# Optimization experiments

Hardware: AMD Instinct MI355X
Metric: run time of the kernel (lower is better)

Reference implementation:

```python
import jax, jax.numpy as jnp
import numpy as np

BATCH, DIN, DSTATE, SEQLEN = 4, 2048, 16, 2048


def setup_inputs() -> dict:
    key = jax.random.key(0)
    ks = jax.random.split(key, 7)
    u = jax.random.normal(ks[0], (BATCH, DIN, SEQLEN), dtype=jnp.float32)
    # delta pre-softplus; moderate positive-ish values like Mamba dt_proj output
    delta = jax.random.uniform(ks[1], (BATCH, DIN, SEQLEN), dtype=jnp.float32, minval=-2.0, maxval=1.0)
    # A is negative in real Mamba (A = -exp(A_log)); keep recurrence stable
    A = -jnp.exp(jax.random.uniform(ks[2], (DIN, DSTATE), dtype=jnp.float32, minval=-1.0, maxval=1.0))
    B = jax.random.normal(ks[3], (BATCH, DSTATE, SEQLEN), dtype=jnp.float32)
    C = jax.random.normal(ks[4], (BATCH, DSTATE, SEQLEN), dtype=jnp.float32)
    D = jax.random.normal(ks[5], (DIN,), dtype=jnp.float32)
    z = jax.random.normal(ks[6], (BATCH, DIN, SEQLEN), dtype=jnp.float32)
    return {"u": u, "delta": delta, "A": A, "B": B, "C": C, "D": D, "z": z}


def reference(u, delta, A, B, C, D, z):
    """Mamba selective scan (selective_scan_ref semantics, delta_softplus=True).

    u, delta, z: (b, d, l); A: (d, n); B, C: (b, n, l); D: (d,).
    y_t = C_t . x_t + D*u_t, x_t = exp(dt_t*A)*x_{t-1} + dt_t*B_t*u_t,
    final y gated by SiLU(z).
    """
    dt = jax.nn.softplus(delta)                      # (b, d, l)

    def step(x, inp):
        dt_t, u_t, B_t, C_t = inp                    # (b,d) (b,d) (b,n) (b,n)
        dA = jnp.exp(dt_t[..., None] * A)            # (b, d, n)
        x = x * dA + (dt_t * u_t)[..., None] * B_t[:, None, :]
        y_t = jnp.einsum('bdn,bn->bd', x, C_t)
        return x, y_t

    xs = (jnp.moveaxis(dt, -1, 0),                   # (l, b, d)
          jnp.moveaxis(u, -1, 0),
          jnp.moveaxis(B, -1, 0),                    # (l, b, n)
          jnp.moveaxis(C, -1, 0))
    x0 = jnp.zeros((u.shape[0], u.shape[1], A.shape[1]), dtype=u.dtype)
    _, ys = jax.lax.scan(step, x0, xs)               # ys: (l, b, d)
    y = jnp.moveaxis(ys, 0, -1)                      # (b, d, l)
    y = y + D[None, :, None] * u
    y = y * (z * jax.nn.sigmoid(z))                  # SiLU gate
    return y
```

## Files before the change

kernel.cpp:

```cpp
#include <hip/hip_runtime.h>


#define BATCHSZ 4
#define DIN 2048
#define NSTATE 16
#define SEQ 2048
#define NCH (BATCHSZ * DIN)
#define NGRP (NCH / 256)
#define TT 32
#define ST 36
#define L2E 1.44269504f

__device__ __forceinline__ float softplus_f(float v) {
    float e = __builtin_amdgcn_exp2f(v * L2E);
    return 0.69314718f * __builtin_amdgcn_logf(1.0f + e);
}

__device__ __forceinline__ float silu_f(float v) {
    float s = __builtin_amdgcn_rcpf(1.0f + __builtin_amdgcn_exp2f(-v * L2E));
    return v * s;
}

__device__ __forceinline__ float comp4(const float4& f, int k) {
    return k == 0 ? f.x : k == 1 ? f.y : k == 2 ? f.z : f.w;
}

__device__ __forceinline__ void set4(float4& f, int k, float v) {
    if (k == 0) f.x = v; else if (k == 1) f.y = v; else if (k == 2) f.z = v; else f.w = v;
}


template<int NC>
__global__ __launch_bounds__(256, 2) void k_pass1(
        const float* __restrict__ u, const float* __restrict__ delta,
        const float* __restrict__ A, const float* __restrict__ Bm,
        float* __restrict__ ws) {
    constexpr int LC = SEQ / NC;
    constexpr int NT = LC / TT;
    __shared__ float Ub[256 * ST];
    __shared__ float Db[256 * ST];
    __shared__ float Bc[LC * 20];

    int tid = threadIdx.x;
    int g = blockIdx.x & (NGRP - 1);
    int c = blockIdx.x >> 5;
    int chBase = g << 8;
    int b = chBase >> 11;
    int bd = chBase + tid;
    int d = bd & (DIN - 1);

    float A2[NSTATE];
    {
        const float* Ar = A + (size_t)d * NSTATE;
        #pragma unroll
        for (int n = 0; n < NSTATE; ++n) A2[n] = Ar[n] * L2E;
    }

    const float* ug = u + (size_t)chBase * SEQ + (size_t)c * LC;
    const float* dg = delta + (size_t)chBase * SEQ + (size_t)c * LC;
    const float* Bg = Bm + (size_t)b * NSTATE * SEQ + (size_t)c * LC;

    #pragma unroll
    for (int i = 0; i < LC * NSTATE / 256; ++i) {
        int e = i * 256 + tid;
        int n = e / LC;
        int t = e % LC;
        Bc[t * 20 + n] = Bg[(size_t)n * SEQ + t];
    }

    float x[NSTATE];
    #pragma unroll
    for (int n = 0; n < NSTATE; ++n) x[n] = 0.0f;
    float S = 0.0f;

    for (int tile = 0; tile < NT; ++tile) {
        int tb = tile * TT;
        __syncthreads();
        #pragma unroll
        for (int it = 0; it < 8; ++it) {
            int r = it * 32 + (tid >> 3), cq = (tid & 7) * 4;
            *(float4*)(&Ub[r * ST + cq]) = *(const float4*)(ug + (size_t)r * SEQ + tb + cq);
            *(float4*)(&Db[r * ST + cq]) = *(const float4*)(dg + (size_t)r * SEQ + tb + cq);
        }
        __syncthreads();
        #pragma unroll
        for (int t4 = 0; t4 < TT / 4; ++t4) {
            float4 u4 = *(const float4*)(&Ub[tid * ST + t4 * 4]);
            float4 d4 = *(const float4*)(&Db[tid * ST + t4 * 4]);
            #pragma unroll
            for (int k = 0; k < 4; ++k) {
                float dt = softplus_f(comp4(d4, k));
                S += dt;
                float du = dt * comp4(u4, k);
                int t = tb + t4 * 4 + k;
                const float4* Br = (const float4*)(&Bc[t * 20]);
                float bb[NSTATE];
                *(float4*)&bb[0] = Br[0]; *(float4*)&bb[4] = Br[1];
                *(float4*)&bb[8] = Br[2]; *(float4*)&bb[12] = Br[3];
                #pragma unroll
                for (int n = 0; n < NSTATE; ++n) {
                    float dA = __builtin_amdgcn_exp2f(A2[n] * dt);
                    x[n] = x[n] * dA + du * bb[n];
                }
            }
        }
    }

    float* wsq = ws;
    float* wsS = ws + (size_t)NSTATE * NC * NCH;
    #pragma unroll
    for (int n = 0; n < NSTATE; ++n) wsq[((size_t)n * NC + c) * NCH + bd] = x[n];
    wsS[(size_t)c * NCH + bd] = S;
}

template<int NC>
__global__ __launch_bounds__(256) void k_pass2(
        const float* __restrict__ A, float* __restrict__ ws) {
    int idx = blockIdx.x * 256 + threadIdx.x;
    int n = idx >> 13;
    int bd = idx & (NCH - 1);
    int d = bd & (DIN - 1);

    float A2 = A[(size_t)d * NSTATE + n] * L2E;
    float x = 0.0f;
    float* wsq = ws;
    float* wsS = ws + (size_t)NSTATE * NC * NCH;

    for (int c = 0; c < NC; ++c) {
        float S = wsS[(size_t)c * NCH + bd];
        float* p = wsq + ((size_t)n * NC + c) * NCH + bd;
        float q = *p;
        float P = __builtin_amdgcn_exp2f(A2 * S);
        *p = x;
        x = x * P + q;
    }
}

template<int NC>
__global__ __launch_bounds__(256, 2) void k_pass3(
        const float* __restrict__ u, const float* __restrict__ delta,
        const float* __restrict__ A, const float* __restrict__ Bm,
        const float* __restrict__ Cm, const float* __restrict__ Dv,
        const float* __restrict__ z, const float* __restrict__ ws,
        float* __restrict__ out) {
    constexpr int LC = SEQ / NC;
    constexpr int NT = LC / TT;
    __shared__ float Ub[256 * ST];
    __shared__ float Db[256 * ST];
    __shared__ float Bc[LC * 20];
    __shared__ float Cc[LC * 20];

    int tid = threadIdx.x;
    int g = blockIdx.x & (NGRP - 1);
    int c = blockIdx.x >> 5;
    int chBase = g << 8;
    int b = chBase >> 11;
    int bd = chBase + tid;
    int d = bd & (DIN - 1);

    float A2[NSTATE];
    {
        const float* Ar = A + (size_t)d * NSTATE;
        #pragma unroll
        for (int n = 0; n < NSTATE; ++n) A2[n] = Ar[n] * L2E;
    }

    const float* ug = u + (size_t)chBase * SEQ + (size_t)c * LC;
    const float* dg = delta + (size_t)chBase * SEQ + (size_t)c * LC;
    const float* zg = z + (size_t)chBase * SEQ + (size_t)c * LC;
    float* og = out + (size_t)chBase * SEQ + (size_t)c * LC;
    const float* Bg = Bm + (size_t)b * NSTATE * SEQ + (size_t)c * LC;
    const float* Cg = Cm + (size_t)b * NSTATE * SEQ + (size_t)c * LC;

    #pragma unroll
    for (int i = 0; i < LC * NSTATE / 256; ++i) {
        int e = i * 256 + tid;
        int n = e / LC;
        int t = e % LC;
        Bc[t * 20 + n] = Bg[(size_t)n * SEQ + t];
        Cc[t * 20 + n] = Cg[(size_t)n * SEQ + t];
    }

    const float* wsq = ws;
    float x[NSTATE];
    #pragma unroll
    for (int n = 0; n < NSTATE; ++n)
        x[n] = wsq[((size_t)n * NC + c) * NCH + bd];
    float Dd = Dv[d];

    for (int tile = 0; tile < NT; ++tile) {
        int tb = tile * TT;
        __syncthreads();
        float4 zr[8];
        #pragma unroll
        for (int it = 0; it < 8; ++it) {
            int r = it * 32 + (tid >> 3), cq = (tid & 7) * 4;
            *(float4*)(&Ub[r * ST + cq]) = *(const float4*)(ug + (size_t)r * SEQ + tb + cq);
            *(float4*)(&Db[r * ST + cq]) = *(const float4*)(dg + (size_t)r * SEQ + tb + cq);
            zr[it] = *(const float4*)(zg + (size_t)r * SEQ + tb + cq);
        }
        __syncthreads();
        #pragma unroll
        for (int t4 = 0; t4 < TT / 4; ++t4) {
            float4 u4 = *(const float4*)(&Ub[tid * ST + t4 * 4]);
            float4 d4 = *(const float4*)(&Db[tid * ST + t4 * 4]);
            float4 y4;
            #pragma unroll
            for (int k = 0; k < 4; ++k) {
                float uv = comp4(u4, k);
                float dt = softplus_f(comp4(d4, k));
                float du = dt * uv;
                int t = tb + t4 * 4 + k;
                const float4* Br = (const float4*)(&Bc[t * 20]);
                const float4* Cr = (const float4*)(&Cc[t * 20]);
                float bb[NSTATE], cc[NSTATE];
                *(float4*)&bb[0] = Br[0]; *(float4*)&bb[4] = Br[1];
                *(float4*)&bb[8] = Br[2]; *(float4*)&bb[12] = Br[3];
                *(float4*)&cc[0] = Cr[0]; *(float4*)&cc[4] = Cr[1];
                *(float4*)&cc[8] = Cr[2]; *(float4*)&cc[12] = Cr[3];
                float acc = 0.0f;
                #pragma unroll
                for (int n = 0; n < NSTATE; ++n) {
                    float dA = __builtin_amdgcn_exp2f(A2[n] * dt);
                    x[n] = x[n] * dA + du * bb[n];
                    acc += x[n] * cc[n];
                }
                set4(y4, k, acc + Dd * uv);
            }
            *(float4*)(&Ub[tid * ST + t4 * 4]) = y4;
        }
        __syncthreads();
        #pragma unroll
        for (int it = 0; it < 8; ++it) {
            int r = it * 32 + (tid >> 3), cq = (tid & 7) * 4;
            float4 y4 = *(const float4*)(&Ub[r * ST + cq]);
            float4 oo;
            #pragma unroll
            for (int k = 0; k < 4; ++k)
                set4(oo, k, comp4(y4, k) * silu_f(comp4(zr[it], k)));
            *(float4*)(og + (size_t)r * SEQ + tb + cq) = oo;
        }
    }
}

__global__ __launch_bounds__(256) void k_simple(
        const float* __restrict__ u, const float* __restrict__ delta,
        const float* __restrict__ A, const float* __restrict__ Bm,
        const float* __restrict__ Cm, const float* __restrict__ Dv,
        const float* __restrict__ z, float* __restrict__ out) {
    int bd = blockIdx.x * 256 + threadIdx.x;
    int b  = bd >> 11;
    int d  = bd & (DIN - 1);

    float A2[NSTATE];
    const float* Ar = A + d * NSTATE;
    #pragma unroll
    for (int n = 0; n < NSTATE; ++n) A2[n] = Ar[n] * L2E;
    float x[NSTATE];
    #pragma unroll
    for (int n = 0; n < NSTATE; ++n) x[n] = 0.0f;

    float Dd = Dv[d];
    size_t base = (size_t)bd * SEQ;
    const float4* u4 = (const float4*)(u + base);
    const float4* d4 = (const float4*)(delta + base);
    const float4* z4 = (const float4*)(z + base);
    float4* o4 = (float4*)(out + base);
    const float* Bp = Bm + (size_t)b * NSTATE * SEQ;
    const float* Cp = Cm + (size_t)b * NSTATE * SEQ;

    for (int t4 = 0; t4 < SEQ / 4; ++t4) {
        float4 uu = u4[t4];
        float4 dd = d4[t4];
        float4 zz = z4[t4];
        float4 yy;
        #pragma unroll
        for (int k = 0; k < 4; ++k) {
            float uv = comp4(uu, k);
            float dt = softplus_f(comp4(dd, k));
            float du = dt * uv;
            int t = t4 * 4 + k;
            float acc = 0.0f;
            #pragma unroll
            for (int n = 0; n < NSTATE; ++n) {
                float dA = __builtin_amdgcn_exp2f(A2[n] * dt);
                x[n] = x[n] * dA + du * Bp[n * SEQ + t];
                acc += x[n] * Cp[n * SEQ + t];
            }
            float y = acc + Dd * uv;
            y = y * silu_f(comp4(zz, k));
            set4(yy, k, y);
        }
        o4[t4] = yy;
    }
}

template<int NC>
static void launch_chunked(const float* u, const float* delta, const float* A,
                           const float* Bm, const float* Cm, const float* Dv,
                           const float* z, float* ws, float* out, hipStream_t stream) {
    k_pass1<NC><<<NGRP * NC, 256, 0, stream>>>(u, delta, A, Bm, ws);
    k_pass2<NC><<<(NSTATE * NCH) / 256, 256, 0, stream>>>(A, ws);
    k_pass3<NC><<<NGRP * NC, 256, 0, stream>>>(u, delta, A, Bm, Cm, Dv, z, ws, out);
}

extern "C" void kernel_launch(void* const* d_in, const int* in_sizes, int n_in,
                              void* d_out, int out_size, void* d_ws, size_t ws_size,
                              hipStream_t stream) {
    const float* u     = (const float*)d_in[0];
    const float* delta = (const float*)d_in[1];
    const float* A     = (const float*)d_in[2];
    const float* Bm    = (const float*)d_in[3];
    const float* Cm    = (const float*)d_in[4];
    const float* Dv    = (const float*)d_in[5];
    const float* z     = (const float*)d_in[6];
    float* out = (float*)d_out;
    float* ws = (float*)d_ws;

    size_t need64 = (size_t)(NSTATE + 1) * 64 * NCH * sizeof(float);
    size_t need32 = (size_t)(NSTATE + 1) * 32 * NCH * sizeof(float);
    size_t need16 = (size_t)(NSTATE + 1) * 16 * NCH * sizeof(float);
    if (ws_size >= need64) {
        launch_chunked<64>(u, delta, A, Bm, Cm, Dv, z, ws, out, stream);
    } else if (ws_size >= need32) {
        launch_chunked<32>(u, delta, A, Bm, Cm, Dv, z, ws, out, stream);
    } else if (ws_size >= need16) {
        launch_chunked<16>(u, delta, A, Bm, Cm, Dv, z, ws, out, stream);
    } else {
        k_simple<<<NCH / 256, 256, 0, stream>>>(u, delta, A, Bm, Cm, Dv, z, out);
    }
}
```

Before: 377.9 us.

## Make tile staging wave-local to drop block barriers; shrink tiles, raise occupancy

Tile loading in pass1 and pass3 now has each 64-thread wavefront stage only its own rows of u/delta/z into LDS, in 16-step subtiles, so the per-tile __syncthreads calls disappear. One barrier remains after the B/C preload. Smaller LDS tiles let launch_bounds rise from 2 to 3 blocks per CU. Pass2 is unrolled by 4 over chunks so more loads are in flight. The risks are higher register pressure at 3 blocks per CU and relying on wavefront-lockstep LDS visibility with no barrier.

```diff
diff --git a/kernel.cpp b/kernel.cpp
--- a/kernel.cpp
+++ b/kernel.cpp
@@ -7,8 +7,8 @@
 #define SEQ 2048
 #define NCH (BATCHSZ * DIN)
 #define NGRP (NCH / 256)
-#define TT 32
-#define ST 36
+#define SUB 16
+#define ST 20
 #define L2E 1.44269504f
 
 __device__ __forceinline__ float softplus_f(float v) {
@@ -31,17 +31,19 @@
 
 
 template<int NC>
-__global__ __launch_bounds__(256, 2) void k_pass1(
+__global__ __launch_bounds__(256, 3) void k_pass1(
         const float* __restrict__ u, const float* __restrict__ delta,
         const float* __restrict__ A, const float* __restrict__ Bm,
-        float* __restrict__ ws) {
+        float* __restrict__ wsq, float* __restrict__ wsS) {
     constexpr int LC = SEQ / NC;
-    constexpr int NT = LC / TT;
+    constexpr int NSUB = LC / SUB;
     __shared__ float Ub[256 * ST];
     __shared__ float Db[256 * ST];
     __shared__ float Bc[LC * 20];
 
     int tid = threadIdx.x;
+    int w6 = tid & ~63;
+    int l = tid & 63;
     int g = blockIdx.x & (NGRP - 1);
     int c = blockIdx.x >> 5;
     int chBase = g << 8;
@@ -49,42 +51,42 @@
     int bd = chBase + tid;
     int d = bd & (DIN - 1);
 
+    const float* ug = u + (size_t)chBase * SEQ + (size_t)c * LC;
+    const float* dg = delta + (size_t)chBase * SEQ + (size_t)c * LC;
+    const float* Bg = Bm + (size_t)b * NSTATE * SEQ + (size_t)c * LC;
+
+    #pragma unroll
+    for (int i = 0; i < LC * NSTATE / 256; ++i) {
+        int e = i * 256 + tid;
+        int n = e / LC;
+        int t = e - n * LC;
+        Bc[t * 20 + n] = Bg[(size_t)n * SEQ + t];
+    }
+
     float A2[NSTATE];
     {
         const float* Ar = A + (size_t)d * NSTATE;
         #pragma unroll
         for (int n = 0; n < NSTATE; ++n) A2[n] = Ar[n] * L2E;
     }
-
-    const float* ug = u + (size_t)chBase * SEQ + (size_t)c * LC;
-    const float* dg = delta + (size_t)chBase * SEQ + (size_t)c * LC;
-    const float* Bg = Bm + (size_t)b * NSTATE * SEQ + (size_t)c * LC;
-
-    #pragma unroll
-    for (int i = 0; i < LC * NSTATE / 256; ++i) {
-        int e = i * 256 + tid;
-        int n = e / LC;
-        int t = e % LC;
-        Bc[t * 20 + n] = Bg[(size_t)n * SEQ + t];
-    }
-
     float x[NSTATE];
     #pragma unroll
     for (int n = 0; n < NSTATE; ++n) x[n] = 0.0f;
     float S = 0.0f;
 
-    for (int tile = 0; tile < NT; ++tile) {
-        int tb = tile * TT;
-        __syncthreads();
-        #pragma unroll
-        for (int it = 0; it < 8; ++it) {
-            int r = it * 32 + (tid >> 3), cq = (tid & 7) * 4;
+    __syncthreads();
+
+    for (int st = 0; st < NSUB; ++st) {
+        int tb = st * SUB;
+        #pragma unroll
+        for (int it = 0; it < 4; ++it) {
+            int r = w6 + it * 16 + (l >> 2);
+            int cq = (l & 3) << 2;
             *(float4*)(&Ub[r * ST + cq]) = *(const float4*)(ug + (size_t)r * SEQ + tb + cq);
             *(float4*)(&Db[r * ST + cq]) = *(const float4*)(dg + (size_t)r * SEQ + tb + cq);
         }
-        __syncthreads();
-        #pragma unroll
-        for (int t4 = 0; t4 < TT / 4; ++t4) {
+        #pragma unroll
+        for (int t4 = 0; t4 < SUB / 4; ++t4) {
             float4 u4 = *(const float4*)(&Ub[tid * ST + t4 * 4]);
             float4 d4 = *(const float4*)(&Db[tid * ST + t4 * 4]);
             #pragma unroll
@@ -106,8 +108,6 @@
         }
     }
 
-    float* wsq = ws;
-    float* wsS = ws + (size_t)NSTATE * NC * NCH;
     #pragma unroll
     for (int n = 0; n < NSTATE; ++n) wsq[((size_t)n * NC + c) * NCH + bd] = x[n];
     wsS[(size_t)c * NCH + bd] = S;
@@ -115,7 +115,8 @@
 
 template<int NC>
 __global__ __launch_bounds__(256) void k_pass2(
-        const float* __restrict__ A, float* __restrict__ ws) {
+        const float* __restrict__ A, float* __restrict__ wsq,
+        float* __restrict__ wsS) {
     int idx = blockIdx.x * 256 + threadIdx.x;
     int n = idx >> 13;
     int bd = idx & (NCH - 1);
@@ -123,34 +124,43 @@
 
     float A2 = A[(size_t)d * NSTATE + n] * L2E;
     float x = 0.0f;
-    float* wsq = ws;
-    float* wsS = ws + (size_t)NSTATE * NC * NCH;
-
-    for (int c = 0; c < NC; ++c) {
-        float S = wsS[(size_t)c * NCH + bd];
-        float* p = wsq + ((size_t)n * NC + c) * NCH + bd;
-        float q = *p;
-        float P = __builtin_amdgcn_exp2f(A2 * S);
-        *p = x;
-        x = x * P + q;
+    float* qbase = wsq + (size_t)n * NC * NCH + bd;
+
+    for (int c0 = 0; c0 < NC; c0 += 4) {
+        float S0 = wsS[(size_t)(c0 + 0) * NCH + bd];
+        float S1 = wsS[(size_t)(c0 + 1) * NCH + bd];
+        float S2 = wsS[(size_t)(c0 + 2) * NCH + bd];
+        float S3 = wsS[(size_t)(c0 + 3) * NCH + bd];
+        float* p0 = qbase + (size_t)(c0 + 0) * NCH;
+        float* p1 = qbase + (size_t)(c0 + 1) * NCH;
+        float* p2 = qbase + (size_t)(c0 + 2) * NCH;
+        float* p3 = qbase + (size_t)(c0 + 3) * NCH;
+        float q0 = *p0, q1 = *p1, q2 = *p2, q3 = *p3;
+        float t0 = x; x = x * __builtin_amdgcn_exp2f(A2 * S0) + q0;
+        float t1 = x; x = x * __builtin_amdgcn_exp2f(A2 * S1) + q1;
+        float t2 = x; x = x * __builtin_amdgcn_exp2f(A2 * S2) + q2;
+        float t3 = x; x = x * __builtin_amdgcn_exp2f(A2 * S3) + q3;
+        *p0 = t0; *p1 = t1; *p2 = t2; *p3 = t3;
     }
 }
 
 template<int NC>
-__global__ __launch_bounds__(256, 2) void k_pass3(
+__global__ __launch_bounds__(256, 3) void k_pass3(
         const float* __restrict__ u, const float* __restrict__ delta,
         const float* __restrict__ A, const float* __restrict__ Bm,
         const float* __restrict__ Cm, const float* __restrict__ Dv,
-        const float* __restrict__ z, const float* __restrict__ ws,
+        const float* __restrict__ z, const float* __restrict__ wsq,
         float* __restrict__ out) {
     constexpr int LC = SEQ / NC;
-    constexpr int NT = LC / TT;
+    constexpr int NSUB = LC / SUB;
     __shared__ float Ub[256 * ST];
     __shared__ float Db[256 * ST];
     __shared__ float Bc[LC * 20];
     __shared__ float Cc[LC * 20];
 
     int tid = threadIdx.x;
+    int w6 = tid & ~63;
+    int l = tid & 63;
     int g = blockIdx.x & (NGRP - 1);
     int c = blockIdx.x >> 5;
     int chBase = g << 8;
@@ -158,13 +168,6 @@
     int bd = chBase + tid;
     int d = bd & (DIN - 1);
 
-    float A2[NSTATE];
-    {
-        const float* Ar = A + (size_t)d * NSTATE;
-        #pragma unroll
-        for (int n = 0; n < NSTATE; ++n) A2[n] = Ar[n] * L2E;
-    }
-
     const float* ug = u + (size_t)chBase * SEQ + (size_t)c * LC;
     const float* dg = delta + (size_t)chBase * SEQ + (size_t)c * LC;
     const float* zg = z + (size_t)chBase * SEQ + (size_t)c * LC;
@@ -176,32 +179,38 @@
     for (int i = 0; i < LC * NSTATE / 256; ++i) {
         int e = i * 256 + tid;
         int n = e / LC;
-        int t = e % LC;
+        int t = e - n * LC;
         Bc[t * 20 + n] = Bg[(size_t)n * SEQ + t];
         Cc[t * 20 + n] = Cg[(size_t)n * SEQ + t];
     }
 
-    const float* wsq = ws;
+    float A2[NSTATE];
+    {
+        const float* Ar = A + (size_t)d * NSTATE;
+        #pragma unroll
+        for (int n = 0; n < NSTATE; ++n) A2[n] = Ar[n] * L2E;
+    }
     float x[NSTATE];
     #pragma unroll
     for (int n = 0; n < NSTATE; ++n)
         x[n] = wsq[((size_t)n * NC + c) * NCH + bd];
     float Dd = Dv[d];
 
-    for (int tile = 0; tile < NT; ++tile) {
-        int tb = tile * TT;
-        __syncthreads();
-        float4 zr[8];
-        #pragma unroll
-        for (int it = 0; it < 8; ++it) {
-            int r = it * 32 + (tid >> 3), cq = (tid & 7) * 4;
+    __syncthreads();
+
+    for (int st = 0; st < NSUB; ++st) {
+        int tb = st * SUB;
+        float4 zr[4];
+        #pragma unroll
+        for (int it = 0; it < 4; ++it) {
+            int r = w6 + it * 16 + (l >> 2);
+            int cq = (l & 3) << 2;
             *(float4*)(&Ub[r * ST + cq]) = *(const float4*)(ug + (size_t)r * SEQ + tb + cq);
             *(float4*)(&Db[r * ST + cq]) = *(const float4*)(dg + (size_t)r * SEQ + tb + cq);
             zr[it] = *(const float4*)(zg + (size_t)r * SEQ + tb + cq);
         }
-        __syncthreads();
-        #pragma unroll
-        for (int t4 = 0; t4 < TT / 4; ++t4) {
+        #pragma unroll
+        for (int t4 = 0; t4 < SUB / 4; ++t4) {
             float4 u4 = *(const float4*)(&Ub[tid * ST + t4 * 4]);
             float4 d4 = *(const float4*)(&Db[tid * ST + t4 * 4]);
             float4 y4;
@@ -229,10 +238,10 @@
             }
             *(float4*)(&Ub[tid * ST + t4 * 4]) = y4;
         }
-        __syncthreads();
-        #pragma unroll
-        for (int it = 0; it < 8; ++it) {
-            int r = it * 32 + (tid >> 3), cq = (tid & 7) * 4;
+        #pragma unroll
+        for (int it = 0; it < 4; ++it) {
+            int r = w6 + it * 16 + (l >> 2);
+            int cq = (l & 3) << 2;
             float4 y4 = *(const float4*)(&Ub[r * ST + cq]);
             float4 oo;
             #pragma unroll
@@ -276,9 +285,9 @@
         float4 yy;
         #pragma unroll
         for (int k = 0; k < 4; ++k) {
-            float uv = comp4(uu, k);
+            float uvk = comp4(uu, k);
             float dt = softplus_f(comp4(dd, k));
-            float du = dt * uv;
+            float du = dt * uvk;
             int t = t4 * 4 + k;
             float acc = 0.0f;
             #pragma unroll
@@ -287,7 +296,7 @@
                 x[n] = x[n] * dA + du * Bp[n * SEQ + t];
                 acc += x[n] * Cp[n * SEQ + t];
             }
-            float y = acc + Dd * uv;
+            float y = acc + Dd * uvk;
             y = y * silu_f(comp4(zz, k));
             set4(yy, k, y);
         }
@@ -299,9 +308,11 @@
 static void launch_chunked(const float* u, const float* delta, const float* A,
                            const float* Bm, const float* Cm, const float* Dv,
                            const float* z, float* ws, float* out, hipStream_t stream) {
-    k_pass1<NC><<<NGRP * NC, 256, 0, stream>>>(u, delta, A, Bm, ws);
-    k_pass2<NC><<<(NSTATE * NCH) / 256, 256, 0, stream>>>(A, ws);
-    k_pass3<NC><<<NGRP * NC, 256, 0, stream>>>(u, delta, A, Bm, Cm, Dv, z, ws, out);
+    float* wsq = ws;
+    float* wsS = ws + (size_t)NSTATE * NC * NCH;
+    k_pass1<NC><<<NGRP * NC, 256, 0, stream>>>(u, delta, A, Bm, wsq, wsS);
+    k_pass2<NC><<<(NSTATE * NCH) / 256, 256, 0, stream>>>(A, wsq, wsS);
+    k_pass3<NC><<<NGRP * NC, 256, 0, stream>>>(u, delta, A, Bm, Cm, Dv, z, wsq, out);
 }
 
 extern "C" void kernel_launch(void* const* d_in, const int* in_sizes, int n_in,
```

New measurement: 369.1 us. 1.02x faster.
